# Kernel tuning notes

Measured on AMD Instinct MI355X. Metric: run time of the kernel, lower is better.

## Reference

```python
import jax, jax.numpy as jnp
import numpy as np


def setup_inputs() -> dict:
    key = jax.random.key(0)
    ks = jax.random.split(key, 10)
    B, L, Din, Dout = 64, 512, 256, 256
    s = 0.05
    inp = jax.random.normal(ks[0], (B, L, Din), jnp.float32)
    ci = jax.random.randint(ks[1], (B, L), 0, L)
    # valid coref indices: ci[:, i] must be in [0, i] (refers to an already-produced state)
    ci = ci % (jnp.arange(L) + 1)[None, :]
    p = lambda k, sh: jax.random.normal(k, sh, jnp.float32) * s
    return {
        "inp": inp,
        "last_coref_idx": ci,
        "Wr": p(ks[2], (Din, Dout)), "br": jnp.zeros((Dout,), jnp.float32),
        "Ur": p(ks[3], (Dout, Dout)),
        "Wz": p(ks[4], (Din, Dout)), "bz": jnp.zeros((Dout,), jnp.float32),
        "Uz": p(ks[5], (Dout, Dout)),
        "Wh": p(ks[6], (Din, Dout)), "bh": jnp.zeros((Dout,), jnp.float32),
        "Uh": p(ks[7], (Dout, Dout)),
        "k1": p(ks[8], (Din, 1)),
        "k2": p(ks[9], (Din, 1)),
    }


def reference(inp, last_coref_idx, Wr, br, Ur, Wz, bz, Uz, Wh, bh, Uh, k1, k2):
    B, L, Din = inp.shape
    Dout = Wr.shape[1]
    split = Dout // 2
    bidx = jnp.arange(B)

    def step(carry, xs):
        h_last, hist = carry            # h_last [B,Dout], hist [L,B,Dout]
        x, c, i = xs                    # x [B,Din], c [B] int, i scalar step index
        # coref = state_history[c-1][b] if c > 0 else zeros
        coref = hist[jnp.clip(c - 1, 0), bidx]
        coref = jnp.where((c > 0)[:, None], coref, jnp.zeros_like(coref))
        # attention between h_last-half and coref-half
        e = jnp.concatenate([x @ k1, x @ k2], axis=1)      # [B,2]
        a = jax.nn.softmax(e, axis=1)[:, 0:1]              # [B,1]
        mt = jnp.concatenate([a * h_last[:, :split], (1.0 - a) * coref[:, split:]], axis=1)
        r = jax.nn.sigmoid(x @ Wr + br + mt @ Ur)
        z = jax.nn.sigmoid(x @ Wz + bz + mt @ Uz)
        h_ = jnp.tanh(x @ Wh + bh + r * (mt @ Uh))
        h = (1.0 - z) * mt + z * h_
        hist = jax.lax.dynamic_update_index_in_dim(hist, h, i, 0)
        return (h, hist), h

    h0 = jnp.zeros((B, Dout), inp.dtype)
    hist0 = jnp.zeros((L, B, Dout), inp.dtype)
    xs = (jnp.swapaxes(inp, 0, 1), jnp.swapaxes(last_coref_idx, 0, 1), jnp.arange(L))
    _, ys = jax.lax.scan(step, (h0, hist0), xs)            # ys [L,B,Dout]
    return jnp.swapaxes(ys, 0, 1)                          # [B,L,Dout]
```

## Files before the change

### kernel.cpp

```cpp
#include <hip/hip_runtime.h>
#include <stdint.h>
#include <stddef.h>

typedef _Float16 half_t;
typedef _Float16 half2_t __attribute__((ext_vector_type(2)));
typedef _Float16 half8_t __attribute__((ext_vector_type(8)));
typedef float    floatx4 __attribute__((ext_vector_type(4)));
typedef uint32_t u32x4   __attribute__((ext_vector_type(4)));
typedef int      intx4   __attribute__((ext_vector_type(4)));

#define SEQ_L 512
#define NBATCH 64
#define DIM 256
#define NTOT (NBATCH * SEQ_L)

__device__ __forceinline__ int dot4i8(uint32_t a, uint32_t b, int c) {
#if defined(__has_builtin)
#if __has_builtin(__builtin_amdgcn_sdot4)
  return __builtin_amdgcn_sdot4((int)a, (int)b, c, false);
#else
  int s = c;
  s += (int)(int8_t)(a)       * (int)(int8_t)(b);
  s += (int)(int8_t)(a >> 8)  * (int)(int8_t)(b >> 8);
  s += (int)(int8_t)(a >> 16) * (int)(int8_t)(b >> 16);
  s += (int)(int8_t)(a >> 24) * (int)(int8_t)(b >> 24);
  return s;
#endif
#else
  int s = c;
  s += (int)(int8_t)(a)       * (int)(int8_t)(b);
  s += (int)(int8_t)(a >> 8)  * (int)(int8_t)(b >> 8);
  s += (int)(int8_t)(a >> 16) * (int)(int8_t)(b >> 16);
  s += (int)(int8_t)(a >> 24) * (int)(int8_t)(b >> 24);
  return s;
#endif
}

__device__ __forceinline__ float sigmoidf_fast(float x) {
  return 1.0f / (1.0f + __expf(-x));
}
__device__ __forceinline__ float tanhf_fast(float x) {
  float e = __expf(2.0f * x);
  return 1.0f - 2.0f / (e + 1.0f);
}

__global__ void conv_w_kernel(const float* __restrict__ Wr,
                              const float* __restrict__ Wz,
                              const float* __restrict__ Wh,
                              half_t* __restrict__ Wt) {
  int n = blockIdx.x;
  int k = threadIdx.x;
  const float* W = (n < 256) ? Wr : ((n < 512) ? Wz : Wh);
  int j = n & 255;
  Wt[(size_t)n * DIM + k] = (half_t)W[(size_t)k * DIM + j];
}

__global__ __launch_bounds__(256) void attn_a_kernel(const float* __restrict__ inp,
                                                     const float* __restrict__ k1,
                                                     const float* __restrict__ k2,
                                                     float* __restrict__ a_arr) {
  int row  = blockIdx.x * 4 + (threadIdx.x >> 6);
  int lane = threadIdx.x & 63;
  const float4* x4 = (const float4*)(inp + (size_t)row * DIM);
  float4 xv  = x4[lane];
  float4 k1v = ((const float4*)k1)[lane];
  float4 k2v = ((const float4*)k2)[lane];
  float e1 = xv.x * k1v.x + xv.y * k1v.y + xv.z * k1v.z + xv.w * k1v.w;
  float e2 = xv.x * k2v.x + xv.y * k2v.y + xv.z * k2v.z + xv.w * k2v.w;
#pragma unroll
  for (int off = 32; off >= 1; off >>= 1) {
    e1 += __shfl_xor(e1, off);
    e2 += __shfl_xor(e2, off);
  }
  if (lane == 0) a_arr[row] = 1.0f / (1.0f + __expf(e2 - e1));
}

__global__ __launch_bounds__(256) void uscale_kernel(const float* __restrict__ Ur,
                                                     const float* __restrict__ Uz,
                                                     const float* __restrict__ Uh,
                                                     float* __restrict__ su) {
  const int g = blockIdx.x;
  const int j = threadIdx.x;
  const float* U = (g == 0) ? Ur : ((g == 1) ? Uz : Uh);
  float m = 0.0f;
  for (int k = 0; k < DIM; ++k) m = fmaxf(m, fabsf(U[(size_t)k * DIM + j]));
  su[g * DIM + j] = fmaxf(m, 1e-30f) * (1.0f / 127.0f);
}

__global__ __launch_bounds__(256) void upack_kernel(const float* __restrict__ Ur,
                                                    const float* __restrict__ Uz,
                                                    const float* __restrict__ Uh,
                                                    const float* __restrict__ su,
                                                    uint32_t* __restrict__ Ui8) {
  const int g = blockIdx.x;
  const int j = threadIdx.x;
  const float* U = (g == 0) ? Ur : ((g == 1) ? Uz : Uh);
  const float r = 1.0f / su[g * DIM + j];
  for (int q = 0; q < 64; ++q) {
    uint32_t w = 0;
#pragma unroll
    for (int t = 0; t < 4; ++t) {
      float v = U[(size_t)(q * 4 + t) * DIM + j] * r;
      int mi = __float2int_rn(v);
      mi = mi < -127 ? -127 : (mi > 127 ? 127 : mi);
      w |= ((uint32_t)(mi & 0xFF)) << (8 * t);
    }
    Ui8[((size_t)g * 64 + q) * DIM + j] = w;
  }
}

__global__ __launch_bounds__(256) void gemm_p_kernel(const float* __restrict__ X,
                                                     const half_t* __restrict__ Wt,
                                                     half_t* __restrict__ P) {
  __shared__ __align__(16) half_t As[128][32];
  __shared__ __align__(16) half_t Bs[128][32];
  const int tid  = threadIdx.x;
  const int bm   = blockIdx.x * 128;
  const int bn   = blockIdx.y * 128;
  const int lane = tid & 63;
  const int wave = tid >> 6;
  const int wm   = (wave >> 1) * 64;
  const int wn   = (wave & 1) * 64;
  const int quad = lane >> 4;
  const int l15  = lane & 15;
  const int r0   = tid >> 2;
  const int kc   = (tid & 3) * 8;

  floatx4 acc[4][4] = {};

  for (int k0 = 0; k0 < DIM; k0 += 32) {
#pragma unroll
    for (int hh = 0; hh < 2; ++hh) {
      int r = r0 + hh * 64;
      const float* asrc = X + (size_t)(bm + r) * DIM + k0 + kc;
      float4 f0 = *(const float4*)(asrc);
      float4 f1 = *(const float4*)(asrc + 4);
      half8_t av;
      av[0] = (half_t)f0.x; av[1] = (half_t)f0.y; av[2] = (half_t)f0.z; av[3] = (half_t)f0.w;
      av[4] = (half_t)f1.x; av[5] = (half_t)f1.y; av[6] = (half_t)f1.z; av[7] = (half_t)f1.w;
      *(half8_t*)(&As[r][kc]) = av;
      *(half8_t*)(&Bs[r][kc]) = *(const half8_t*)(Wt + (size_t)(bn + r) * DIM + k0 + kc);
    }
    __syncthreads();
    half8_t af[4], bf[4];
#pragma unroll
    for (int mi = 0; mi < 4; ++mi)
      af[mi] = *(const half8_t*)(&As[wm + mi * 16 + l15][quad * 8]);
#pragma unroll
    for (int ni = 0; ni < 4; ++ni)
      bf[ni] = *(const half8_t*)(&Bs[wn + ni * 16 + l15][quad * 8]);
#pragma unroll
    for (int mi = 0; mi < 4; ++mi)
#pragma unroll
      for (int ni = 0; ni < 4; ++ni)
        acc[mi][ni] = __builtin_amdgcn_mfma_f32_16x16x32_f16(af[mi], bf[ni], acc[mi][ni], 0, 0, 0);
    __syncthreads();
  }
#pragma unroll
  for (int mi = 0; mi < 4; ++mi)
#pragma unroll
    for (int ni = 0; ni < 4; ++ni) {
      int col = bn + wn + ni * 16 + l15;
#pragma unroll
      for (int rr = 0; rr < 4; ++rr) {
        int row = bm + wm + mi * 16 + quad * 4 + rr;
        P[(size_t)row * 768 + col] = (half_t)acc[mi][ni][rr];
      }
    }
}

__global__ __launch_bounds__(512, 2) void recur_kernel(
    const half_t* __restrict__ P,
    const float* __restrict__ a_arr,
    const int* __restrict__ cidx,
    const uint32_t* __restrict__ Ui8,
    const float* __restrict__ su,
    const float* __restrict__ br, const float* __restrict__ bz, const float* __restrict__ bh,
    float* __restrict__ out) {
  const int tid  = threadIdx.x;
  const int j    = tid >> 1;
  const int half = tid & 1;

  __shared__ __align__(16) half_t   hist[SEQ_L][128];
  __shared__ __align__(16) uint32_t mtb[2][64];

  u32x4 ur8[8], uz8[8], uh8[8];
#pragma unroll
  for (int c8 = 0; c8 < 8; ++c8) {
#pragma unroll
    for (int t = 0; t < 4; ++t) {
      const int quad = half * 32 + c8 * 4 + t;
      ur8[c8][t] = Ui8[((size_t)0 * 64 + quad) * DIM + j];
      uz8[c8][t] = Ui8[((size_t)1 * 64 + quad) * DIM + j];
      uh8[c8][t] = Ui8[((size_t)2 * 64 + quad) * DIM + j];
    }
  }
#pragma unroll
  for (int c8 = 0; c8 < 8; ++c8) {
    asm volatile("" : "+v"(ur8[c8]), "+v"(uz8[c8]), "+v"(uh8[c8]));
  }

  const float scr = su[0 * DIM + j] * (1.0f / 127.0f);
  const float scz = su[1 * DIM + j] * (1.0f / 127.0f);
  const float sch = su[2 * DIM + j] * (1.0f / 127.0f);
  const float brj = br[j], bzj = bz[j], bhj = bh[j];

  if (tid < 64) mtb[0][tid] = 0u;

  float mtj = 0.0f;
  const int base = blockIdx.x * SEQ_L;

  const half_t* prow0 = P + (size_t)base * 768;
  float pr_c = (float)prow0[j];
  float pz_c = (float)prow0[DIM + j];
  float ph_c = (float)prow0[2 * DIM + j];
  float a_n = a_arr[base + 1];
  int   c_n = cidx[base + 1];

  __syncthreads();

  for (int i = 0; i < SEQ_L; ++i) {
    const int ip1 = (i + 1 < SEQ_L) ? (i + 1) : i;
    const half_t* prow = P + (size_t)(base + ip1) * 768;
    float pr_x = (float)prow[j];
    float pz_x = (float)prow[DIM + j];
    float ph_x = (float)prow[2 * DIM + j];
    const int ip2 = (i + 2 < SEQ_L) ? (i + 2) : (SEQ_L - 1);
    const float a_x = a_arr[base + ip2];
    const int   c_x = cidx[base + ip2];

    const int  cp    = c_n - 1;
    const bool use_h = (cp == i);
    float corefv = 0.0f;
    if (j >= 128) {
      if (c_n > 0 && !use_h) corefv = (float)hist[cp][j - 128];
    }

    int ar = 0, az = 0, ah = 0;
    const u32x4* mq = (const u32x4*)(&mtb[i & 1][half * 32]);
#pragma unroll
    for (int c8 = 0; c8 < 8; ++c8) {
      u32x4 m4 = mq[c8];
      ar = dot4i8(m4.x, ur8[c8][0], ar);
      az = dot4i8(m4.x, uz8[c8][0], az);
      ah = dot4i8(m4.x, uh8[c8][0], ah);
      ar = dot4i8(m4.y, ur8[c8][1], ar);
      az = dot4i8(m4.y, uz8[c8][1], az);
      ah = dot4i8(m4.y, uh8[c8][1], ah);
      ar = dot4i8(m4.z, ur8[c8][2], ar);
      az = dot4i8(m4.z, uz8[c8][2], az);
      ah = dot4i8(m4.z, uh8[c8][2], ah);
      ar = dot4i8(m4.w, ur8[c8][3], ar);
      az = dot4i8(m4.w, uz8[c8][3], az);
      ah = dot4i8(m4.w, uh8[c8][3], ah);
    }
    ar += __shfl_xor(ar, 1);
    az += __shfl_xor(az, 1);
    ah += __shfl_xor(ah, 1);

    const float fr = (float)ar * scr;
    const float fz = (float)az * scz;
    const float fh = (float)ah * sch;
    const float rg = sigmoidf_fast(pr_c + brj + fr);
    const float zg = sigmoidf_fast(pz_c + bzj + fz);
    const float hb = tanhf_fast(ph_c + bhj + rg * fh);
    const float h  = (1.0f - zg) * mtj + zg * hb;

    if (tid & 1) {
      out[(size_t)(base + i) * DIM + j] = h;
      if (j >= 128) hist[i][j - 128] = (half_t)h;
    }

    float mtn;
    if (j < 128) {
      mtn = a_n * h;
    } else {
      const float coref = (c_n > 0) ? (use_h ? h : corefv) : 0.0f;
      mtn = (1.0f - a_n) * coref;
    }
    mtj = mtn;

    int mi = __float2int_rn(mtn * 127.0f);
    mi = mi < -127 ? -127 : (mi > 127 ? 127 : mi);
    unsigned v0 = (unsigned)mi & 0xFFu;
    unsigned o1 = (unsigned)__shfl_xor((int)v0, 2) & 0xFFu;
    unsigned pp = (j & 1) ? (o1 | (v0 << 8)) : (v0 | (o1 << 8));
    unsigned o2 = (unsigned)__shfl_xor((int)pp, 4);
    unsigned qd = (j & 2) ? ((o2 & 0xFFFFu) | (pp << 16))
                          : ((pp & 0xFFFFu) | (o2 << 16));
    if ((tid & 7) == 0) mtb[(i + 1) & 1][j >> 2] = qd;

    pr_c = pr_x; pz_c = pz_x; ph_c = ph_x;
    a_n = a_x;   c_n = c_x;

    __syncthreads();
  }
}

extern "C" void kernel_launch(void* const* d_in, const int* in_sizes, int n_in,
                              void* d_out, int out_size, void* d_ws, size_t ws_size,
                              hipStream_t stream) {
  const float* inp = (const float*)d_in[0];
  const int*   ci  = (const int*)d_in[1];
  const float* Wr  = (const float*)d_in[2];
  const float* br  = (const float*)d_in[3];
  const float* Ur  = (const float*)d_in[4];
  const float* Wz  = (const float*)d_in[5];
  const float* bz  = (const float*)d_in[6];
  const float* Uz  = (const float*)d_in[7];
  const float* Wh  = (const float*)d_in[8];
  const float* bh  = (const float*)d_in[9];
  const float* Uh  = (const float*)d_in[10];
  const float* k1  = (const float*)d_in[11];
  const float* k2  = (const float*)d_in[12];
  float* out = (float*)d_out;

  char* ws = (char*)d_ws;
  half_t*   Wt    = (half_t*)ws;
  half_t*   P     = (half_t*)(ws + 393216);
  float*    a_arr = (float*)(ws + 393216 + 50331648);
  float*    su    = (float*)(ws + 50855936);
  uint32_t* Ui8   = (uint32_t*)(ws + 50859008);

  conv_w_kernel<<<dim3(768), dim3(256), 0, stream>>>(Wr, Wz, Wh, Wt);
  attn_a_kernel<<<dim3(NTOT / 4), dim3(256), 0, stream>>>(inp, k1, k2, a_arr);
  uscale_kernel<<<dim3(3), dim3(256), 0, stream>>>(Ur, Uz, Uh, su);
  upack_kernel<<<dim3(3), dim3(256), 0, stream>>>(Ur, Uz, Uh, su, Ui8);
  gemm_p_kernel<<<dim3(NTOT / 128, 6), dim3(256), 0, stream>>>(inp, Wt, P);
  recur_kernel<<<dim3(NBATCH), dim3(512), 0, stream>>>(P, a_arr, ci, Ui8, su,
                                                       br, bz, bh, out);
}
```

Measured before the change: 753.6 us.

## Split recurrence dot products over four lanes and batch output stores via LDS ring

```diff
diff --git a/kernel.cpp b/kernel.cpp
--- a/kernel.cpp
+++ b/kernel.cpp
@@ -169,7 +169,7 @@
     }
 }
 
-__global__ __launch_bounds__(512, 2) void recur_kernel(
+__global__ __launch_bounds__(1024, 4) void recur_kernel(
     const half_t* __restrict__ P,
     const float* __restrict__ a_arr,
     const int* __restrict__ cidx,
@@ -177,27 +177,24 @@
     const float* __restrict__ su,
     const float* __restrict__ br, const float* __restrict__ bz, const float* __restrict__ bh,
     float* __restrict__ out) {
-  const int tid  = threadIdx.x;
-  const int j    = tid >> 1;
-  const int half = tid & 1;
+  const int tid = threadIdx.x;
+  const int j   = tid >> 2;
+  const int q   = tid & 3;
 
   __shared__ __align__(16) half_t   hist[SEQ_L][128];
+  __shared__ __align__(16) float    ring[16][DIM];
   __shared__ __align__(16) uint32_t mtb[2][64];
 
-  u32x4 ur8[8], uz8[8], uh8[8];
-#pragma unroll
-  for (int c8 = 0; c8 < 8; ++c8) {
+  u32x4 ur4[4], uz4[4], uh4[4];
+#pragma unroll
+  for (int c = 0; c < 4; ++c) {
 #pragma unroll
     for (int t = 0; t < 4; ++t) {
-      const int quad = half * 32 + c8 * 4 + t;
-      ur8[c8][t] = Ui8[((size_t)0 * 64 + quad) * DIM + j];
-      uz8[c8][t] = Ui8[((size_t)1 * 64 + quad) * DIM + j];
-      uh8[c8][t] = Ui8[((size_t)2 * 64 + quad) * DIM + j];
-    }
-  }
-#pragma unroll
-  for (int c8 = 0; c8 < 8; ++c8) {
-    asm volatile("" : "+v"(ur8[c8]), "+v"(uz8[c8]), "+v"(uh8[c8]));
+      const int quad = q * 16 + c * 4 + t;
+      ur4[c][t] = Ui8[((size_t)0 * 64 + quad) * DIM + j];
+      uz4[c][t] = Ui8[((size_t)1 * 64 + quad) * DIM + j];
+      uh4[c][t] = Ui8[((size_t)2 * 64 + quad) * DIM + j];
+    }
   }
 
   const float scr = su[0 * DIM + j] * (1.0f / 127.0f);
@@ -220,6 +217,26 @@
   __syncthreads();
 
   for (int i = 0; i < SEQ_L; ++i) {
+    asm volatile("" : "+v"(ur4[0]), "+v"(ur4[1]), "+v"(ur4[2]), "+v"(ur4[3]));
+    asm volatile("" : "+v"(uz4[0]), "+v"(uz4[1]), "+v"(uz4[2]), "+v"(uz4[3]));
+    asm volatile("" : "+v"(uh4[0]), "+v"(uh4[1]), "+v"(uh4[2]), "+v"(uh4[3]));
+
+    if ((i & 7) == 0 && i > 0) {
+#pragma unroll
+      for (int p = 0; p < 2; ++p) {
+        const int e   = p * 1024 + tid;
+        const int row = i - 8 + (e >> 8);
+        out[(size_t)(base + row) * DIM + (e & 255)] = ring[row & 15][e & 255];
+      }
+    }
+
+    const int  cp    = c_n - 1;
+    const bool use_h = (cp == i);
+    float corefv = 0.0f;
+    if (j >= 128) {
+      if (c_n > 0 && !use_h) corefv = (float)hist[cp][j - 128];
+    }
+
     const int ip1 = (i + 1 < SEQ_L) ? (i + 1) : i;
     const half_t* prow = P + (size_t)(base + ip1) * 768;
     float pr_x = (float)prow[j];
@@ -229,34 +246,26 @@
     const float a_x = a_arr[base + ip2];
     const int   c_x = cidx[base + ip2];
 
-    const int  cp    = c_n - 1;
-    const bool use_h = (cp == i);
-    float corefv = 0.0f;
-    if (j >= 128) {
-      if (c_n > 0 && !use_h) corefv = (float)hist[cp][j - 128];
-    }
-
     int ar = 0, az = 0, ah = 0;
-    const u32x4* mq = (const u32x4*)(&mtb[i & 1][half * 32]);
-#pragma unroll
-    for (int c8 = 0; c8 < 8; ++c8) {
-      u32x4 m4 = mq[c8];
-      ar = dot4i8(m4.x, ur8[c8][0], ar);
-      az = dot4i8(m4.x, uz8[c8][0], az);
-      ah = dot4i8(m4.x, uh8[c8][0], ah);
-      ar = dot4i8(m4.y, ur8[c8][1], ar);
-      az = dot4i8(m4.y, uz8[c8][1], az);
-      ah = dot4i8(m4.y, uh8[c8][1], ah);
-      ar = dot4i8(m4.z, ur8[c8][2], ar);
-      az = dot4i8(m4.z, uz8[c8][2], az);
-      ah = dot4i8(m4.z, uh8[c8][2], ah);
-      ar = dot4i8(m4.w, ur8[c8][3], ar);
-      az = dot4i8(m4.w, uz8[c8][3], az);
-      ah = dot4i8(m4.w, uh8[c8][3], ah);
-    }
-    ar += __shfl_xor(ar, 1);
-    az += __shfl_xor(az, 1);
-    ah += __shfl_xor(ah, 1);
+    const u32x4* mq = (const u32x4*)(&mtb[i & 1][q * 16]);
+#pragma unroll
+    for (int c = 0; c < 4; ++c) {
+      u32x4 m4 = mq[c];
+      ar = dot4i8(m4.x, ur4[c][0], ar);
+      az = dot4i8(m4.x, uz4[c][0], az);
+      ah = dot4i8(m4.x, uh4[c][0], ah);
+      ar = dot4i8(m4.y, ur4[c][1], ar);
+      az = dot4i8(m4.y, uz4[c][1], az);
+      ah = dot4i8(m4.y, uh4[c][1], ah);
+      ar = dot4i8(m4.z, ur4[c][2], ar);
+      az = dot4i8(m4.z, uz4[c][2], az);
+      ah = dot4i8(m4.z, uh4[c][2], ah);
+      ar = dot4i8(m4.w, ur4[c][3], ar);
+      az = dot4i8(m4.w, uz4[c][3], az);
+      ah = dot4i8(m4.w, uh4[c][3], ah);
+    }
+    ar += __shfl_xor(ar, 1);  az += __shfl_xor(az, 1);  ah += __shfl_xor(ah, 1);
+    ar += __shfl_xor(ar, 2);  az += __shfl_xor(az, 2);  ah += __shfl_xor(ah, 2);
 
     const float fr = (float)ar * scr;
     const float fz = (float)az * scz;
@@ -266,8 +275,8 @@
     const float hb = tanhf_fast(ph_c + bhj + rg * fh);
     const float h  = (1.0f - zg) * mtj + zg * hb;
 
-    if (tid & 1) {
-      out[(size_t)(base + i) * DIM + j] = h;
+    if (q == 3) {
+      ring[i & 15][j] = h;
       if (j >= 128) hist[i][j - 128] = (half_t)h;
     }
 
@@ -283,17 +292,24 @@
     int mi = __float2int_rn(mtn * 127.0f);
     mi = mi < -127 ? -127 : (mi > 127 ? 127 : mi);
     unsigned v0 = (unsigned)mi & 0xFFu;
-    unsigned o1 = (unsigned)__shfl_xor((int)v0, 2) & 0xFFu;
+    unsigned o1 = (unsigned)__shfl_xor((int)v0, 4) & 0xFFu;
     unsigned pp = (j & 1) ? (o1 | (v0 << 8)) : (v0 | (o1 << 8));
-    unsigned o2 = (unsigned)__shfl_xor((int)pp, 4);
+    unsigned o2 = (unsigned)__shfl_xor((int)pp, 8);
     unsigned qd = (j & 2) ? ((o2 & 0xFFFFu) | (pp << 16))
                           : ((pp & 0xFFFFu) | (o2 << 16));
-    if ((tid & 7) == 0) mtb[(i + 1) & 1][j >> 2] = qd;
+    if ((tid & 15) == 0) mtb[(i + 1) & 1][j >> 2] = qd;
 
     pr_c = pr_x; pz_c = pz_x; ph_c = ph_x;
     a_n = a_x;   c_n = c_x;
 
     __syncthreads();
+  }
+
+#pragma unroll
+  for (int p = 0; p < 2; ++p) {
+    const int e   = p * 1024 + tid;
+    const int row = 504 + (e >> 8);
+    out[(size_t)(base + row) * DIM + (e & 255)] = ring[row & 15][e & 255];
   }
 }
 
@@ -327,6 +343,6 @@
   uscale_kernel<<<dim3(3), dim3(256), 0, stream>>>(Ur, Uz, Uh, su);
   upack_kernel<<<dim3(3), dim3(256), 0, stream>>>(Ur, Uz, Uh, su, Ui8);
   gemm_p_kernel<<<dim3(NTOT / 128, 6), dim3(256), 0, stream>>>(inp, Wt, P);
-  recur_kernel<<<dim3(NBATCH), dim3(512), 0, stream>>>(P, a_arr, ci, Ui8, su,
-                                                       br, bz, bh, out);
-}
+  recur_kernel<<<dim3(NBATCH), dim3(1024), 0, stream>>>(P, a_arr, ci, Ui8, su,
+                                                        br, bz, bh, out);
+}
```

New measurement: 907.0 us. 20.4% more time.
